# Kernel optimization log

Hardware: AMD Instinct MI355X
Metric: run time of the kernel (lower is better)

## Reference

```python
import jax, jax.numpy as jnp
import numpy as np

B, N, D = 1, 2048, 1024
H = 16
HD = D // H
MAX_REL = 100          # relative_positional_distance
NUM_EMB = 2 * MAX_REL - 1
NEG = 1e8


def _rel_pos_logits(q_pos, rel_emb):
    """Fairseq-style learned relative positional logits (unmasked).

    q_pos:   [L, B*H, hd]  (unscaled queries)
    rel_emb: [H, 2*MAX_REL-1, hd]
    returns: [B*H, L, L]
    """
    L = q_pos.shape[0]
    pad_len = max(L - MAX_REL, 0)
    start = max(MAX_REL - L, 0)
    # get_embeddings_for_query: pad to cover relative offsets -(L-1)..(L-1)
    padded = jnp.pad(rel_emb, ((0, 0), (pad_len, pad_len), (0, 0)))
    used = padded[:, start:start + 2 * L - 1, :]          # [H, 2L-1, hd]
    # calculate_positional_logits
    q4 = q_pos.reshape(L, -1, H, HD)                       # [L, B, H, hd]
    logits = jnp.einsum('lbhd,hmd->lbhm', q4, used)        # [L, B, H, 2L-1]
    logits = logits.reshape(L, -1, 2 * L - 1)              # [L, BH, 2L-1]
    if pad_len > 0:  # mask relative positions beyond max_relative_pos
        logits = logits.at[:, :, :pad_len].add(-NEG)
        logits = logits.at[:, :, -pad_len:].add(-NEG)
    # relative_to_absolute_indexing (unmasked skewing trick)
    bh = logits.shape[1]
    x = jnp.pad(logits, ((0, 0), (0, 0), (0, 1)))          # [L, BH, 2L]
    x = jnp.transpose(x, (1, 0, 2)).reshape(bh, L * 2 * L)
    x = jnp.pad(x, ((0, 0), (0, L - 1)))
    x = x.reshape(bh, L + 1, 2 * L - 1)
    return x[:, :L, L - 1:]                                # [BH, L, L]


def setup_inputs() -> dict:
    key = jax.random.key(0)
    ks = jax.random.split(key, 6)
    x = jax.random.normal(ks[0], (B, N, D), dtype=jnp.float32)
    qkv_w = jax.random.normal(ks[1], (3 * D, D), dtype=jnp.float32) * 0.02
    qkv_b = jnp.zeros((3 * D,), dtype=jnp.float32)
    proj_w = jax.random.normal(ks[2], (D, D), dtype=jnp.float32) * 0.02
    proj_b = jnp.zeros((D,), dtype=jnp.float32)
    rel_emb = jax.random.normal(ks[3], (H, NUM_EMB, HD), dtype=jnp.float32) * (HD ** -0.5)
    return {"x": x, "qkv_w": qkv_w, "qkv_b": qkv_b,
            "proj_w": proj_w, "proj_b": proj_b, "rel_emb": rel_emb}


def reference(x, qkv_w, qkv_b, proj_w, proj_b, rel_emb):
    b, n, d = x.shape
    qkv = x @ qkv_w.T + qkv_b                                # [B,N,3D]
    qkv = qkv.reshape(b, n, 3, H, HD).transpose(2, 0, 3, 1, 4)
    q, k, v = qkv[0], qkv[1], qkv[2]                          # [B,H,N,hd]
    scale = 1.0 / np.sqrt(HD).astype(np.float32)
    logits = jnp.einsum('bhqd,bhkd->bhqk', q, k) * scale      # [B,H,N,N]
    q_pos = jnp.transpose(q, (0, 2, 1, 3)).reshape(n, b * H, HD)
    pos = _rel_pos_logits(q_pos, rel_emb).reshape(b, H, n, n)
    probs = jax.nn.softmax(logits + pos, axis=-1)             # dropout off (eval)
    out = jnp.einsum('bhqk,bhkd->bhqd', probs, v)
    out = jnp.transpose(out, (0, 2, 1, 3)).reshape(b, n, d)
    return out @ proj_w.T + proj_b
```

## Files before the change

kernel.cpp:

```cpp
#include <hip/hip_runtime.h>
#include <hip/hip_bf16.h>

#define N_SEQ 2048
#define DMODEL 1024
#define NHEAD 16
#define HD 64
#define NREL 199

typedef __bf16 bf16x8 __attribute__((ext_vector_type(8)));
typedef float f32x4 __attribute__((ext_vector_type(4)));

__device__ __forceinline__ bf16x8 cvt8(float4 a, float4 b) {
    bf16x8 r;
    r[0] = (__bf16)a.x; r[1] = (__bf16)a.y; r[2] = (__bf16)a.z; r[3] = (__bf16)a.w;
    r[4] = (__bf16)b.x; r[5] = (__bf16)b.y; r[6] = (__bf16)b.z; r[7] = (__bf16)b.w;
    return r;
}

#define MFMA16(A, B, C) __builtin_amdgcn_mfma_f32_16x16x32_bf16(A, B, C, 0, 0, 0)

__device__ __forceinline__ void async_copy16(void* lds, const void* g) {
    __builtin_amdgcn_global_load_lds(
        (__attribute__((address_space(1))) unsigned int*)g,
        (__attribute__((address_space(3))) unsigned int*)lds, 16, 0, 0);
}

__global__ __launch_bounds__(256) void cvt3(
    const float* __restrict__ a, __bf16* __restrict__ ao, int na,
    const float* __restrict__ b, __bf16* __restrict__ bo, int nb,
    const float* __restrict__ c, __bf16* __restrict__ co)
{
    int i = (blockIdx.x * blockDim.x + threadIdx.x) * 8;
    const float* src; __bf16* dst;
    if (i < na)              { src = a + i;            dst = ao + i; }
    else if (i - na < nb)    { src = b + (i - na);     dst = bo + (i - na); }
    else                     { src = c + (i - na - nb); dst = co + (i - na - nb); }
    float4 f0 = ((const float4*)src)[0];
    float4 f1 = ((const float4*)src)[1];
    *(bf16x8*)dst = cvt8(f0, f1);
}

template<int BM, int BN, int KS, bool OUT_BF16>
__global__ __launch_bounds__(256) void gemm_bt64(
    const __bf16* __restrict__ A,
    const __bf16* __restrict__ W,
    const float* __restrict__ bias,
    void* __restrict__ Cout,
    int lda, int Nc, int K, int ldc)
{
    constexpr int RT = BM + BN;
    constexpr int WM = BM / 2, WN = BN / 2;
    constexpr int MI = WM / 16, NI = WN / 16;
    constexpr int CHUNKS = RT / 4 / 8;

    __shared__ __bf16 s[KS][RT][64];

    const int tid  = threadIdx.x;
    const int wid  = tid >> 6;
    const int lane = tid & 63;
    const int quad = lane >> 4;
    const int l15  = lane & 15;
    const int wm   = (wid >> 1) * WM;
    const int wn   = (wid & 1) * WN;
    const int bm   = blockIdx.y * BM;
    const int bn   = blockIdx.x * BN;

    const int lrow = lane >> 3;
    const int lcb  = ((lane & 7) ^ lrow) * 8;

    f32x4 acc[MI][NI] = {};

    for (int k0 = 0; k0 < K; k0 += 64 * KS) {
        #pragma unroll
        for (int ks = 0; ks < KS; ks++)
            #pragma unroll
            for (int c = 0; c < CHUNKS; c++) {
                const int r0 = wid * (RT / 4) + c * 8;
                const __bf16* src = (r0 < BM)
                    ? A + (size_t)(bm + r0 + lrow) * lda + k0 + ks * 64 + lcb
                    : W + (size_t)(bn + (r0 - BM) + lrow) * K + k0 + ks * 64 + lcb;
                async_copy16(&s[ks][r0][0], src);
            }
        __syncthreads();

        #pragma unroll
        for (int ks = 0; ks < KS; ks++)
            #pragma unroll
            for (int half = 0; half < 2; half++) {
                bf16x8 af[MI], bfr[NI];
                #pragma unroll
                for (int mi = 0; mi < MI; mi++) {
                    int ar = wm + mi * 16 + l15;
                    af[mi] = *(const bf16x8*)&s[ks][ar][((quad + 4 * half) ^ (ar & 7)) * 8];
                }
                #pragma unroll
                for (int ni = 0; ni < NI; ni++) {
                    int br = BM + wn + ni * 16 + l15;
                    bfr[ni] = *(const bf16x8*)&s[ks][br][((quad + 4 * half) ^ (br & 7)) * 8];
                }
                #pragma unroll
                for (int mi = 0; mi < MI; mi++)
                    #pragma unroll
                    for (int ni = 0; ni < NI; ni++)
                        acc[mi][ni] = MFMA16(af[mi], bfr[ni], acc[mi][ni]);
            }
        __syncthreads();
    }

    #pragma unroll
    for (int ni = 0; ni < NI; ni++) {
        int col = bn + wn + ni * 16 + l15;
        float bv = bias[col];
        #pragma unroll
        for (int mi = 0; mi < MI; mi++)
            #pragma unroll
            for (int ri = 0; ri < 4; ri++) {
                int row = bm + wm + mi * 16 + quad * 4 + ri;
                float v = acc[mi][ni][ri] + bv;
                if (OUT_BF16)
                    reinterpret_cast<__bf16*>(Cout)[(size_t)row * ldc + col] = (__bf16)v;
                else
                    reinterpret_cast<float*>(Cout)[(size_t)row * ldc + col] = v;
            }
    }
}

__global__ __launch_bounds__(256) void attn_band_mfma(
    __hip_bfloat16* __restrict__ qkv,
    const float* __restrict__ rel_emb)
{
    __shared__ __align__(16) char smem[53248];
    __bf16 (*q_s)[72]   = (__bf16(*)[72])smem;
    __bf16 (*p_s)[72]   = (__bf16(*)[72])smem;
    __bf16 (*P_s)[200]  = (__bf16(*)[200])(smem + 9216);
    __bf16 (*relc)[72]  = (__bf16(*)[72])(smem + 34816);
    __bf16 (*k_s)[72]   = (__bf16(*)[72])(smem + 34816);
    __bf16 (*v_s)[72]   = (__bf16(*)[72])(smem + 34816 + 9216);

    const int tid  = threadIdx.x;
    const int wid  = tid >> 6;
    const int lane = tid & 63;
    const int quad = lane >> 4;
    const int l15  = lane & 15;
    const int h    = blockIdx.x >> 5;
    const int q0   = (blockIdx.x & 31) * 64;
    const int srow = tid >> 2;
    const int sq   = (tid & 3) * 16;

    const int j_lo   = (q0 - 99 > 0) ? (q0 - 99) : 0;
    const int j_hi   = (q0 + 162 < N_SEQ - 1) ? (q0 + 162) : (N_SEQ - 1);
    const int ntiles = (j_hi - j_lo + 64) >> 6;

    uint4 kr0, kr1, vr0, vr1;
    {
        int jr = j_lo + srow; if (jr > N_SEQ - 1) jr = N_SEQ - 1;
        const uint4* ks = (const uint4*)(qkv + (size_t)jr * 3072 + 1024 + h * HD + sq);
        kr0 = ks[0]; kr1 = ks[1];
        const uint4* vs = (const uint4*)(qkv + (size_t)jr * 3072 + 2048 + h * HD + sq);
        vr0 = vs[0]; vr1 = vs[1];
    }

    {
        const __hip_bfloat16* src = qkv + (size_t)(q0 + srow) * 3072 + h * HD + sq;
        uint4 u0 = ((const uint4*)src)[0];
        uint4 u1 = ((const uint4*)src)[1];
        *(uint4*)&q_s[srow][sq]     = u0;
        *(uint4*)&q_s[srow][sq + 8] = u1;
    }
    for (int idx = tid; idx < 112 * 4; idx += 256) {
        int er = idx >> 2, ec = (idx & 3) * 16;
        const float4* s = (const float4*)(rel_emb + ((size_t)h * NREL + er) * HD + ec);
        float4 f0 = s[0], f1 = s[1], f2 = s[2], f3 = s[3];
        *(bf16x8*)&relc[er][ec]     = cvt8(f0, f1);
        *(bf16x8*)&relc[er][ec + 8] = cvt8(f2, f3);
    }
    __syncthreads();

    const bf16x8 aq0 = *(const bf16x8*)&q_s[wid * 16 + l15][quad * 8];
    const bf16x8 aq1 = *(const bf16x8*)&q_s[wid * 16 + l15][quad * 8 + 32];

    #pragma unroll
    for (int t = 0; t < 7; t++) {
        f32x4 pacc = {};
        bf16x8 b0 = *(const bf16x8*)&relc[t * 16 + l15][quad * 8];
        bf16x8 b1 = *(const bf16x8*)&relc[t * 16 + l15][quad * 8 + 32];
        pacc = MFMA16(aq0, b0, pacc);
        pacc = MFMA16(aq1, b1, pacc);
        #pragma unroll
        for (int ri = 0; ri < 4; ri++)
            P_s[wid * 16 + quad * 4 + ri][t * 16 + l15] = (__bf16)pacc[ri];
    }
    __syncthreads();

    for (int idx = tid; idx < 96 * 4; idx += 256) {
        int er = 112 + (idx >> 2); if (er > NREL - 1) er = NREL - 1;
        int ec = (idx & 3) * 16;
        const float4* s = (const float4*)(rel_emb + ((size_t)h * NREL + er) * HD + ec);
        float4 f0 = s[0], f1 = s[1], f2 = s[2], f3 = s[3];
        *(bf16x8*)&relc[idx >> 2][ec]     = cvt8(f0, f1);
        *(bf16x8*)&relc[idx >> 2][ec + 8] = cvt8(f2, f3);
    }
    __syncthreads();

    #pragma unroll
    for (int t = 7; t < 13; t++) {
        f32x4 pacc = {};
        bf16x8 b0 = *(const bf16x8*)&relc[t * 16 + l15 - 112][quad * 8];
        bf16x8 b1 = *(const bf16x8*)&relc[t * 16 + l15 - 112][quad * 8 + 32];
        pacc = MFMA16(aq0, b0, pacc);
        pacc = MFMA16(aq1, b1, pacc);
        #pragma unroll
        for (int ri = 0; ri < 4; ri++) {
            int col = t * 16 + l15;
            if (col < NREL)
                P_s[wid * 16 + quad * 4 + ri][col] = (__bf16)pacc[ri];
        }
    }

    bf16x8 bones;
    {
        __bf16 o = (l15 == 0) ? (__bf16)1.0f : (__bf16)0.0f;
        #pragma unroll
        for (int i = 0; i < 8; i++) bones[i] = o;
    }

    f32x4 O[4] = {};
    f32x4 Osum = {};

    for (int t = 0; t < ntiles; t++) {
        __syncthreads();

        *(uint4*)&k_s[srow][sq]     = kr0;
        *(uint4*)&k_s[srow][sq + 8] = kr1;
        {
            __bf16 vtmp[16];
            *(uint4*)&vtmp[0] = vr0; *(uint4*)&vtmp[8] = vr1;
            #pragma unroll
            for (int i = 0; i < 16; i++) v_s[sq + i][srow] = vtmp[i];
        }
        __syncthreads();

        if (t + 1 < ntiles) {
            int jr = j_lo + (t + 1) * 64 + srow; if (jr > N_SEQ - 1) jr = N_SEQ - 1;
            const uint4* ks = (const uint4*)(qkv + (size_t)jr * 3072 + 1024 + h * HD + sq);
            kr0 = ks[0]; kr1 = ks[1];
            const uint4* vs = (const uint4*)(qkv + (size_t)jr * 3072 + 2048 + h * HD + sq);
            vr0 = vs[0]; vr1 = vs[1];
        }

        const int j0 = j_lo + t * 64;

        f32x4 S[4] = {};
        #pragma unroll
        for (int nt = 0; nt < 4; nt++) {
            bf16x8 b0 = *(const bf16x8*)&k_s[nt * 16 + l15][quad * 8];
            bf16x8 b1 = *(const bf16x8*)&k_s[nt * 16 + l15][quad * 8 + 32];
            S[nt] = MFMA16(aq0, b0, S[nt]);
            S[nt] = MFMA16(aq1, b1, S[nt]);
        }

        #pragma unroll
        for (int nt = 0; nt < 4; nt++) {
            int jg = j0 + nt * 16 + l15;
            #pragma unroll
            for (int ri = 0; ri < 4; ri++) {
                int r_loc = wid * 16 + quad * 4 + ri;
                int e = jg - (q0 + r_loc) + 99;
                float v = -3.0e38f;
                if ((unsigned)e < (unsigned)NREL && jg < N_SEQ)
                    v = S[nt][ri] * 0.125f + (float)P_s[r_loc][e];
                float p = __expf(v);
                p_s[r_loc][nt * 16 + l15] = (__bf16)p;
            }
        }

        bf16x8 ap0 = *(const bf16x8*)&p_s[wid * 16 + l15][quad * 8];
        bf16x8 ap1 = *(const bf16x8*)&p_s[wid * 16 + l15][quad * 8 + 32];
        #pragma unroll
        for (int nt = 0; nt < 4; nt++) {
            bf16x8 b0 = *(const bf16x8*)&v_s[nt * 16 + l15][quad * 8];
            bf16x8 b1 = *(const bf16x8*)&v_s[nt * 16 + l15][quad * 8 + 32];
            O[nt] = MFMA16(ap0, b0, O[nt]);
            O[nt] = MFMA16(ap1, b1, O[nt]);
        }
        Osum = MFMA16(ap0, bones, Osum);
        Osum = MFMA16(ap1, bones, Osum);
    }

    #pragma unroll
    for (int ri = 0; ri < 4; ri++) {
        float s = __shfl(Osum[ri], (lane & 48), 64);
        float inv = 1.0f / s;
        #pragma unroll
        for (int nt = 0; nt < 4; nt++) {
            int r = q0 + wid * 16 + quad * 4 + ri;
            qkv[(size_t)r * 3072 + h * HD + nt * 16 + l15] =
                __float2bfloat16(O[nt][ri] * inv);
        }
    }
}

extern "C" void kernel_launch(void* const* d_in, const int* in_sizes, int n_in,
                              void* d_out, int out_size, void* d_ws, size_t ws_size,
                              hipStream_t stream)
{
    (void)out_size; (void)ws_size; (void)n_in;

    const float *x = nullptr, *qkv_w = nullptr, *qkv_b = nullptr;
    const float *proj_w = nullptr, *proj_b = nullptr, *rel = nullptr;
    for (int i = 0; i < 6; i++) {
        switch (in_sizes[i]) {
            case 2097152: x      = (const float*)d_in[i]; break;
            case 3145728: qkv_w  = (const float*)d_in[i]; break;
            case 3072:    qkv_b  = (const float*)d_in[i]; break;
            case 1048576: proj_w = (const float*)d_in[i]; break;
            case 1024:    proj_b = (const float*)d_in[i]; break;
            case 203776:  rel    = (const float*)d_in[i]; break;
            default: break;
        }
    }

    char* ws = (char*)d_ws;
    __hip_bfloat16* qkv = (__hip_bfloat16*)ws;
    __bf16* xb  = (__bf16*)(ws + 12582912);
    __bf16* wb  = (__bf16*)(ws + 16777216);
    __bf16* pwb = (__bf16*)(ws + 23068672);
    float* out = (float*)d_out;

    cvt3<<<dim3(6291456 / 8 / 256), 256, 0, stream>>>(
        x, xb, 2097152, qkv_w, wb, 3145728, proj_w, pwb);
    gemm_bt64<128, 64, 2, true><<<dim3(3072 / 64, N_SEQ / 128), 256, 0, stream>>>(
        xb, wb, qkv_b, (void*)qkv, DMODEL, 3072, DMODEL, 3072);
    attn_band_mfma<<<dim3(NHEAD * (N_SEQ / 64)), 256, 0, stream>>>(qkv, rel);
    gemm_bt64<64, 64, 2, false><<<dim3(DMODEL / 64, N_SEQ / 64), 256, 0, stream>>>(
        (const __bf16*)qkv, pwb, proj_b, (void*)out, 3072, DMODEL, DMODEL, DMODEL);
}
```

Baseline: 127.3 us.

## Double-buffer LDS tiles in the bf16 GEMMs to overlap loads with MFMA

Replaces the GEMM's two-stage K unroll, which loaded both stages and then computed, with a ping-pong LDS buffer. The async global-to-LDS copy of the next 64-wide K tile is issued before the MFMAs on the current tile. This is meant to hide global load latency behind matrix math in both the QKV and output projection GEMMs. It uses one barrier per 64-wide K step instead of two per 128-wide step. Correctness relies on the barrier at the top of each iteration waiting for the outstanding async loads.

```diff
diff --git a/kernel.cpp b/kernel.cpp
--- a/kernel.cpp
+++ b/kernel.cpp
@@ -40,8 +40,8 @@
     *(bf16x8*)dst = cvt8(f0, f1);
 }
 
-template<int BM, int BN, int KS, bool OUT_BF16>
-__global__ __launch_bounds__(256) void gemm_bt64(
+template<int BM, int BN, bool OUT_BF16>
+__global__ __launch_bounds__(256) void gemm_db(
     const __bf16* __restrict__ A,
     const __bf16* __restrict__ W,
     const float* __restrict__ bias,
@@ -53,7 +53,7 @@
     constexpr int MI = WM / 16, NI = WN / 16;
     constexpr int CHUNKS = RT / 4 / 8;
 
-    __shared__ __bf16 s[KS][RT][64];
+    __shared__ __bf16 s[2][RT][64];
 
     const int tid  = threadIdx.x;
     const int wid  = tid >> 6;
@@ -70,41 +70,43 @@
 
     f32x4 acc[MI][NI] = {};
 
-    for (int k0 = 0; k0 < K; k0 += 64 * KS) {
-        #pragma unroll
-        for (int ks = 0; ks < KS; ks++)
-            #pragma unroll
-            for (int c = 0; c < CHUNKS; c++) {
-                const int r0 = wid * (RT / 4) + c * 8;
-                const __bf16* src = (r0 < BM)
-                    ? A + (size_t)(bm + r0 + lrow) * lda + k0 + ks * 64 + lcb
-                    : W + (size_t)(bn + (r0 - BM) + lrow) * K + k0 + ks * 64 + lcb;
-                async_copy16(&s[ks][r0][0], src);
+    auto stage = [&](int buf, int k0) {
+        #pragma unroll
+        for (int c = 0; c < CHUNKS; c++) {
+            const int r0 = wid * (RT / 4) + c * 8;
+            const __bf16* src = (r0 < BM)
+                ? A + (size_t)(bm + r0 + lrow) * lda + k0 + lcb
+                : W + (size_t)(bn + (r0 - BM) + lrow) * K + k0 + lcb;
+            async_copy16(&s[buf][r0][0], src);
+        }
+    };
+
+    stage(0, 0);
+    int cur = 0;
+    for (int k0 = 0; k0 < K; k0 += 64) {
+        __syncthreads();
+        if (k0 + 64 < K) stage(cur ^ 1, k0 + 64);
+
+        #pragma unroll
+        for (int half = 0; half < 2; half++) {
+            bf16x8 af[MI], bfr[NI];
+            #pragma unroll
+            for (int mi = 0; mi < MI; mi++) {
+                int ar = wm + mi * 16 + l15;
+                af[mi] = *(const bf16x8*)&s[cur][ar][((quad + 4 * half) ^ (ar & 7)) * 8];
             }
-        __syncthreads();
-
-        #pragma unroll
-        for (int ks = 0; ks < KS; ks++)
-            #pragma unroll
-            for (int half = 0; half < 2; half++) {
-                bf16x8 af[MI], bfr[NI];
+            #pragma unroll
+            for (int ni = 0; ni < NI; ni++) {
+                int br = BM + wn + ni * 16 + l15;
+                bfr[ni] = *(const bf16x8*)&s[cur][br][((quad + 4 * half) ^ (br & 7)) * 8];
+            }
+            #pragma unroll
+            for (int mi = 0; mi < MI; mi++)
                 #pragma unroll
-                for (int mi = 0; mi < MI; mi++) {
-                    int ar = wm + mi * 16 + l15;
-                    af[mi] = *(const bf16x8*)&s[ks][ar][((quad + 4 * half) ^ (ar & 7)) * 8];
-                }
-                #pragma unroll
-                for (int ni = 0; ni < NI; ni++) {
-                    int br = BM + wn + ni * 16 + l15;
-                    bfr[ni] = *(const bf16x8*)&s[ks][br][((quad + 4 * half) ^ (br & 7)) * 8];
-                }
-                #pragma unroll
-                for (int mi = 0; mi < MI; mi++)
-                    #pragma unroll
-                    for (int ni = 0; ni < NI; ni++)
-                        acc[mi][ni] = MFMA16(af[mi], bfr[ni], acc[mi][ni]);
-            }
-        __syncthreads();
+                for (int ni = 0; ni < NI; ni++)
+                    acc[mi][ni] = MFMA16(af[mi], bfr[ni], acc[mi][ni]);
+        }
+        cur ^= 1;
     }
 
     #pragma unroll
@@ -329,9 +331,9 @@
 
     cvt3<<<dim3(6291456 / 8 / 256), 256, 0, stream>>>(
         x, xb, 2097152, qkv_w, wb, 3145728, proj_w, pwb);
-    gemm_bt64<128, 64, 2, true><<<dim3(3072 / 64, N_SEQ / 128), 256, 0, stream>>>(
+    gemm_db<128, 64, true><<<dim3(3072 / 64, N_SEQ / 128), 256, 0, stream>>>(
         xb, wb, qkv_b, (void*)qkv, DMODEL, 3072, DMODEL, 3072);
     attn_band_mfma<<<dim3(NHEAD * (N_SEQ / 64)), 256, 0, stream>>>(qkv, rel);
-    gemm_bt64<64, 64, 2, false><<<dim3(DMODEL / 64, N_SEQ / 64), 256, 0, stream>>>(
+    gemm_db<64, 64, false><<<dim3(DMODEL / 64, N_SEQ / 64), 256, 0, stream>>>(
         (const __bf16*)qkv, pwb, proj_b, (void*)out, 3072, DMODEL, DMODEL, DMODEL);
 }
```

Measured after the change: 126.4 us. No clear change (-0.7%).
